# Kernel optimization log

Measured on AMD Instinct MI355X. Metric: run time of the kernel, lower is better.

## Reference

```python
import jax, jax.numpy as jnp
import numpy as np

ALPHA = 1.702
LIMIT = 7.0

# Tiling: A*B*M = BD*S (total dispatched tokens)
A, B, E, M, H, I = 2, 8, 16, 128, 2048, 2048
_BD, _S = 2, 1024


def setup_inputs() -> dict:
    key = jax.random.key(0)
    ks = jax.random.split(key, 6)
    inv_h = 1.0 / np.sqrt(H)
    inv_i = 1.0 / np.sqrt(I)
    return {
        "dispatched": jax.random.normal(ks[0], (A, B, E, M, H), dtype=jnp.float32),
        "gate_up_proj": jax.random.normal(ks[1], (E, H, 2 * I), dtype=jnp.float32) * inv_h,
        "gate_up_proj_bias": jax.random.normal(ks[2], (E, 2 * I), dtype=jnp.float32) * 0.02,
        "down_proj": jax.random.normal(ks[3], (E, I, H), dtype=jnp.float32) * inv_i,
        "down_proj_bias": jax.random.normal(ks[4], (E, H), dtype=jnp.float32) * 0.02,
        "sparsity_remap": jax.random.randint(ks[5], (E, E), 0, E, dtype=jnp.int32),
        "BD": _BD,
        "S": _S,
    }


def _moe_activation_gpt_oss(gate_up_out):
    # interleaved gate/up: [g0,u0,g1,u1,...]
    gate = gate_up_out[..., ::2]
    up = gate_up_out[..., 1::2]
    gate = jnp.minimum(gate, LIMIT)
    up = jnp.clip(up, -LIMIT, LIMIT)
    glu = gate * jax.nn.sigmoid(gate * ALPHA)
    return (up + 1.0) * glu


def reference(dispatched, gate_up_proj, gate_up_proj_bias, down_proj,
              down_proj_bias, sparsity_remap, BD, S):
    # sparsity_remap is an opaque tile remap for tt.sparse_matmul; the dense
    # grouped matmul computes the same math (zero tiles contribute zeros).
    a, b, e, m, h = dispatched.shape
    inter = gate_up_proj.shape[-1] // 2
    # grouped gate_up GEMM: [A,B,E,M,H] @ [E,H,2I] -> [A,B,E,M,2I]
    gate_up_out = jnp.einsum('abemh,ehn->abemn', dispatched, gate_up_proj)
    gate_up_out = gate_up_out + gate_up_proj_bias[None, None, :, None, :]
    activated = _moe_activation_gpt_oss(gate_up_out)  # [A,B,E,M,I]
    activated = activated.reshape(a * b, e, m, inter)
    # grouped down GEMM: [AB,E,M,I] @ [E,I,H] -> [AB,E,M,H]
    down_out = jnp.einsum('xemi,eih->xemh', activated, down_proj)
    down_out = down_out + down_proj_bias[None, :, None, :]
    # untile: [AB,E,M,H] -> [AB,M,E,H] -> [BD,S,E,H]
    down_out = jnp.transpose(down_out, (0, 2, 1, 3))
    return down_out.reshape(BD, S, e, h)
```

## Files before the change

### kernel.cpp

```cpp
#include <hip/hip_runtime.h>
#include <stdint.h>

#define DEV __device__ __forceinline__

constexpr int E_ = 16, M_ = 128, H_ = 2048, I_ = 2048;
constexpr int X_ = 16;
constexpr int N1 = 2 * I_;
constexpr int ROWS = X_ * M_;

typedef short bfrag __attribute__((ext_vector_type(8)));
typedef float ffrag __attribute__((ext_vector_type(4)));
typedef unsigned short us8 __attribute__((ext_vector_type(8)));

DEV unsigned short f2bf(float f) {
    union { float f; unsigned u; } v; v.f = f;
    unsigned u = v.u;
    u += 0x7fffu + ((u >> 16) & 1u);
    return (unsigned short)(u >> 16);
}

DEV void gload16(const void* g, void* lds_wave_base) {
    __builtin_amdgcn_global_load_lds(
        (const __attribute__((address_space(1))) unsigned int*)g,
        (__attribute__((address_space(3))) unsigned int*)lds_wave_base,
        16, 0, 0);
}

DEV void block_bar() {
    asm volatile("" ::: "memory");
    __builtin_amdgcn_s_barrier();
    asm volatile("" ::: "memory");
}


__global__ __launch_bounds__(256) void convert_a(const float* __restrict__ in,
                                                 unsigned short* __restrict__ outb) {
    const int n4 = X_ * E_ * M_ * H_ / 4;
    int idx = blockIdx.x * 256 + threadIdx.x;
    int stride = gridDim.x * 256;
    for (int f = idx; f < n4; f += stride) {
        float4 v = ((const float4*)in)[f];
        ushort4 o;
        o.x = f2bf(v.x); o.y = f2bf(v.y); o.z = f2bf(v.z); o.w = f2bf(v.w);
        const int c = f & 511;
        const int row = f >> 9;
        const int m = row & 127, e = (row >> 7) & 15, x = row >> 11;
        ((ushort4*)outb)[((size_t)(e * ROWS + x * M_ + m) << 9) + c] = o;
    }
}

__global__ __launch_bounds__(256) void convert_b1(const float* __restrict__ gup,
                                                  unsigned short* __restrict__ b1t) {
    const int e = blockIdx.x, h0 = blockIdx.y * 64, n0 = blockIdx.z * 128;
    __shared__ float tile[64][129];
    const float* src = gup + (size_t)e * H_ * N1;
    const int t = threadIdx.x;
#pragma unroll
    for (int i = 0; i < 8; ++i) {
        int idx = i * 1024 + t * 4;
        int r = idx >> 7, c = idx & 127;
        float4 v = *(const float4*)(src + (size_t)(h0 + r) * N1 + n0 + c);
        tile[r][c] = v.x; tile[r][c + 1] = v.y; tile[r][c + 2] = v.z; tile[r][c + 3] = v.w;
    }
    __syncthreads();
    const int p = t >> 2;
    const int hh = (t & 3) * 16;
    us8 g0, g1, u0, u1;
#pragma unroll
    for (int k = 0; k < 8; ++k) {
        g0[k] = f2bf(tile[hh + k][2 * p]);
        u0[k] = f2bf(tile[hh + k][2 * p + 1]);
        g1[k] = f2bf(tile[hh + 8 + k][2 * p]);
        u1[k] = f2bf(tile[hh + 8 + k][2 * p + 1]);
    }
    unsigned short* dg = b1t + ((size_t)e * N1 + (n0 >> 1) + p) * H_ + h0 + hh;
    unsigned short* du = b1t + ((size_t)e * N1 + I_ + (n0 >> 1) + p) * H_ + h0 + hh;
    *(us8*)dg = g0; *(us8*)(dg + 8) = g1;
    *(us8*)du = u0; *(us8*)(du + 8) = u1;
}

__global__ __launch_bounds__(256) void convert_b2(const float* __restrict__ dwn,
                                                  unsigned short* __restrict__ b2t) {
    const int e = blockIdx.x, i0 = blockIdx.y * 64, h0 = blockIdx.z * 64;
    __shared__ float tile[64][65];
    const float* src = dwn + (size_t)e * I_ * H_;
    const int t = threadIdx.x;
#pragma unroll
    for (int it = 0; it < 4; ++it) {
        int idx = it * 1024 + t * 4;
        int r = idx >> 6, c = idx & 63;
        float4 v = *(const float4*)(src + (size_t)(i0 + r) * H_ + h0 + c);
        tile[r][c] = v.x; tile[r][c + 1] = v.y; tile[r][c + 2] = v.z; tile[r][c + 3] = v.w;
    }
    __syncthreads();
    const int hl = t >> 2, ii = (t & 3) * 16;
    us8 o0, o1;
#pragma unroll
    for (int k = 0; k < 8; ++k) {
        o0[k] = f2bf(tile[ii + k][hl]);
        o1[k] = f2bf(tile[ii + 8 + k][hl]);
    }
    unsigned short* d = b2t + ((size_t)e * H_ + h0 + hl) * I_ + i0 + ii;
    *(us8*)d = o0; *(us8*)(d + 8) = o1;
}

template <int MODE>
__global__ __launch_bounds__(512, 2) void gemm8p(
    const unsigned short* __restrict__ A,
    const unsigned short* __restrict__ B,
    const float* __restrict__ bias,
    void* __restrict__ outv)
{
    constexpr int LD = 2048;
    constexpr int BK = 32;
    constexpr int NT = 2048 / BK;

    __shared__ unsigned short lds[4][2][256 * BK];

    const int t = threadIdx.x, wave = t >> 6, lane = t & 63;
    const int wr = wave >> 2, wc = wave & 3;

    int id = blockIdx.x;
    const int cpx = gridDim.x >> 3;
    id = (id & 7) * cpx + (id >> 3);
    int e, mt, bt;
    if (MODE == 0) { e = id >> 7; mt = (id >> 4) & 7; bt = id & 15; }
    else           { e = id >> 6; mt = (id >> 3) & 7; bt = id & 7; }

    const unsigned short* Aexp = A + ((size_t)e * ROWS + mt * 256) * LD;
    const unsigned short* Bexp = (MODE == 0)
        ? B + (size_t)e * N1 * LD
        : B + ((size_t)e * H_ + bt * 256) * LD;

    ffrag acc[8][4];
#pragma unroll
    for (int i = 0; i < 8; ++i)
#pragma unroll
        for (int j = 0; j < 4; ++j) acc[i][j] = ffrag{0.f, 0.f, 0.f, 0.f};

    const int rsub = lane >> 2;
    const int csw = ((lane & 3) ^ ((lane >> 3) & 3)) * 8;

    auto stage = [&](int kt, int b) {
        const int k0 = kt * BK;
#pragma unroll
        for (int i = 0; i < 2; ++i) {
            const int Rb = (wave * 2 + i) * 16;
            const int r = Rb + rsub;
            gload16(Aexp + (size_t)r * LD + k0 + csw, (void*)&lds[b][0][Rb * BK]);
        }
#pragma unroll
        for (int i = 0; i < 2; ++i) {
            const int Rb = (wave * 2 + i) * 16;
            const int r = Rb + rsub;
            int grow;
            if (MODE == 0)
                grow = ((r >> 5) & 1) * I_ + bt * 128 + (r >> 6) * 32 + (r & 31);
            else
                grow = r;
            gload16(Bexp + (size_t)grow * LD + k0 + csw, (void*)&lds[b][1][Rb * BK]);
        }
    };

    stage(0, 0);
    stage(1, 1);
    stage(2, 2);

    const int l15 = lane & 15, lr16 = lane >> 4;
    const int swl = (l15 >> 1) & 3;
    const int kch = (lr16 ^ swl) * 8;
    const int arow0 = wr * 128 + l15;
    const int brow0 = wc * 64 + l15;

#pragma unroll 4
    for (int kt = 0; kt < NT; ++kt) {
        const int cur = kt & 3;

        if (kt + 2 < NT)      { asm volatile("s_waitcnt vmcnt(8)" ::: "memory"); }
        else if (kt + 1 < NT) { asm volatile("s_waitcnt vmcnt(4)" ::: "memory"); }
        else                  { asm volatile("s_waitcnt vmcnt(0)" ::: "memory"); }
        __builtin_amdgcn_sched_barrier(0);
        block_bar();

        bfrag bB[4], af[8];

#pragma unroll
        for (int nf = 0; nf < 4; ++nf)
            bB[nf] = *(const bfrag*)&lds[cur][1][(brow0 + nf * 16) * BK + kch];
#pragma unroll
        for (int mf = 0; mf < 4; ++mf)
            af[mf] = *(const bfrag*)&lds[cur][0][(arow0 + mf * 16) * BK + kch];
        asm volatile("" ::: "memory");
#pragma unroll
        for (int mf = 4; mf < 8; ++mf)
            af[mf] = *(const bfrag*)&lds[cur][0][(arow0 + mf * 16) * BK + kch];

        if (kt + 3 < NT) stage(kt + 3, (kt + 3) & 3);

        asm volatile("s_waitcnt lgkmcnt(4)" ::: "memory");
        __builtin_amdgcn_sched_barrier(0);
        __builtin_amdgcn_s_setprio(1);
#pragma unroll
        for (int mf = 0; mf < 4; ++mf)
#pragma unroll
            for (int nf = 0; nf < 4; ++nf)
                acc[mf][nf] = __builtin_amdgcn_mfma_f32_16x16x32_bf16(
                    af[mf], bB[nf], acc[mf][nf], 0, 0, 0);
        __builtin_amdgcn_s_setprio(0);

        asm volatile("s_waitcnt lgkmcnt(0)" ::: "memory");
        __builtin_amdgcn_sched_barrier(0);
        __builtin_amdgcn_s_setprio(1);
#pragma unroll
        for (int mf = 4; mf < 8; ++mf)
#pragma unroll
            for (int nf = 0; nf < 4; ++nf)
                acc[mf][nf] = __builtin_amdgcn_mfma_f32_16x16x32_bf16(
                    af[mf], bB[nf], acc[mf][nf], 0, 0, 0);
        __builtin_amdgcn_s_setprio(0);
    }

    const int rb = mt * 256 + wr * 128 + lr16 * 4;
    if (MODE == 0) {
        unsigned short* act = (unsigned short*)outv + (size_t)e * ROWS * I_;
#pragma unroll
        for (int nf = 0; nf < 2; ++nf) {
            const int jj = bt * 128 + wc * 32 + nf * 16 + l15;
            const float gb = bias[(size_t)e * N1 + 2 * jj];
            const float ub = bias[(size_t)e * N1 + 2 * jj + 1];
#pragma unroll
            for (int mf = 0; mf < 8; ++mf)
#pragma unroll
                for (int r = 0; r < 4; ++r) {
                    float g = acc[mf][nf][r] + gb;
                    float u = acc[mf][2 + nf][r] + ub;
                    g = fminf(g, 7.0f);
                    u = fminf(fmaxf(u, -7.0f), 7.0f);
                    const float glu = g / (1.0f + __expf(-1.702f * g));
                    const float av = (u + 1.0f) * glu;
                    act[(size_t)(rb + mf * 16 + r) * I_ + jj] = f2bf(av);
                }
        }
    } else {
        float* out = (float*)outv;
#pragma unroll
        for (int nf = 0; nf < 4; ++nf) {
            const int h = bt * 256 + wc * 64 + nf * 16 + l15;
            const float bb = bias[(size_t)e * H_ + h];
#pragma unroll
            for (int mf = 0; mf < 8; ++mf)
#pragma unroll
                for (int r = 0; r < 4; ++r) {
                    const int row = rb + mf * 16 + r;
                    out[((size_t)row * E_ + e) * H_ + h] = acc[mf][nf][r] + bb;
                }
        }
    }
}


extern "C" void kernel_launch(void* const* d_in, const int* in_sizes, int n_in,
                              void* d_out, int out_size, void* d_ws, size_t ws_size,
                              hipStream_t stream) {
    const float* disp  = (const float*)d_in[0];
    const float* gup   = (const float*)d_in[1];
    const float* gub   = (const float*)d_in[2];
    const float* down  = (const float*)d_in[3];
    const float* dbias = (const float*)d_in[4];
    float* out = (float*)d_out;

    const size_t NEED = (size_t)512 << 20;
    if (ws_size < NEED) {
        hipMemsetAsync(d_out, 0, (size_t)out_size * sizeof(float), stream);
        return;
    }
    unsigned short* a_bf = (unsigned short*)d_ws;
    unsigned short* b1t  = (unsigned short*)((char*)d_ws + ((size_t)128 << 20));
    unsigned short* b2t  = b1t;
    unsigned short* actb = (unsigned short*)((char*)d_ws + ((size_t)384 << 20));

    convert_a<<<4096, 256, 0, stream>>>(disp, a_bf);
    convert_b1<<<dim3(E_, H_ / 64, N1 / 128), 256, 0, stream>>>(gup, b1t);
    gemm8p<0><<<2048, 512, 0, stream>>>(a_bf, b1t, gub, actb);
    convert_b2<<<dim3(E_, I_ / 64, H_ / 64), 256, 0, stream>>>(down, b2t);
    gemm8p<1><<<1024, 512, 0, stream>>>(actb, b2t, dbias, out);
}
```

Measured before the change: 1.185 ms.

## Software-pipeline LDS fragment loads across K tiles with ping-pong registers

Restructures the GEMM main loop so that the B fragments and the first half of the A fragments for the next K tile are read from LDS while the current tile's second MFMA half is running. Two register sets alternate between tiles, and the barrier and the next global stage move to the middle of each tile. The goal is to hide LDS read latency behind MFMA work. The cost is higher register pressure, and the loop is unrolled by two, which assumes NT is even.

```diff
diff --git a/kernel.cpp b/kernel.cpp
--- a/kernel.cpp
+++ b/kernel.cpp
@@ -162,63 +162,78 @@
         }
     };
 
-    stage(0, 0);
-    stage(1, 1);
-    stage(2, 2);
-
     const int l15 = lane & 15, lr16 = lane >> 4;
     const int swl = (l15 >> 1) & 3;
     const int kch = (lr16 ^ swl) * 8;
     const int arow0 = wr * 128 + l15;
     const int brow0 = wc * 64 + l15;
 
-#pragma unroll 4
-    for (int kt = 0; kt < NT; ++kt) {
-        const int cur = kt & 3;
-
-        if (kt + 2 < NT)      { asm volatile("s_waitcnt vmcnt(8)" ::: "memory"); }
-        else if (kt + 1 < NT) { asm volatile("s_waitcnt vmcnt(4)" ::: "memory"); }
-        else                  { asm volatile("s_waitcnt vmcnt(0)" ::: "memory"); }
-        __builtin_amdgcn_sched_barrier(0);
-        block_bar();
-
-        bfrag bB[4], af[8];
-
-#pragma unroll
-        for (int nf = 0; nf < 4; ++nf)
-            bB[nf] = *(const bfrag*)&lds[cur][1][(brow0 + nf * 16) * BK + kch];
-#pragma unroll
-        for (int mf = 0; mf < 4; ++mf)
-            af[mf] = *(const bfrag*)&lds[cur][0][(arow0 + mf * 16) * BK + kch];
-        asm volatile("" ::: "memory");
-#pragma unroll
-        for (int mf = 4; mf < 8; ++mf)
-            af[mf] = *(const bfrag*)&lds[cur][0][(arow0 + mf * 16) * BK + kch];
-
-        if (kt + 3 < NT) stage(kt + 3, (kt + 3) & 3);
-
-        asm volatile("s_waitcnt lgkmcnt(4)" ::: "memory");
-        __builtin_amdgcn_sched_barrier(0);
-        __builtin_amdgcn_s_setprio(1);
-#pragma unroll
-        for (int mf = 0; mf < 4; ++mf)
-#pragma unroll
-            for (int nf = 0; nf < 4; ++nf)
-                acc[mf][nf] = __builtin_amdgcn_mfma_f32_16x16x32_bf16(
-                    af[mf], bB[nf], acc[mf][nf], 0, 0, 0);
-        __builtin_amdgcn_s_setprio(0);
-
-        asm volatile("s_waitcnt lgkmcnt(0)" ::: "memory");
-        __builtin_amdgcn_sched_barrier(0);
-        __builtin_amdgcn_s_setprio(1);
-#pragma unroll
-        for (int mf = 4; mf < 8; ++mf)
-#pragma unroll
-            for (int nf = 0; nf < 4; ++nf)
-                acc[mf][nf] = __builtin_amdgcn_mfma_f32_16x16x32_bf16(
-                    af[mf], bB[nf], acc[mf][nf], 0, 0, 0);
-        __builtin_amdgcn_s_setprio(0);
-    }
+    bfrag bB_a[4], af_a[4], bB_b[4], af_b[4];
+
+    stage(0, 0);
+    stage(1, 1);
+    stage(2, 2);
+    asm volatile("s_waitcnt vmcnt(8)" ::: "memory");
+    __builtin_amdgcn_sched_barrier(0);
+    block_bar();
+#pragma unroll
+    for (int nf = 0; nf < 4; ++nf)
+        bB_a[nf] = *(const bfrag*)&lds[0][1][(brow0 + nf * 16) * BK + kch];
+#pragma unroll
+    for (int mf = 0; mf < 4; ++mf)
+        af_a[mf] = *(const bfrag*)&lds[0][0][(arow0 + mf * 16) * BK + kch];
+
+#define TILE_BODY(KT_, BBC, A03C, BBN, A03N)                                     \
+  {                                                                              \
+    const int kt_ = (KT_);                                                       \
+    const int cur_ = kt_ & 3;                                                    \
+    asm volatile("s_waitcnt lgkmcnt(0)" ::: "memory");      \
+    __builtin_amdgcn_sched_barrier(0);                                           \
+    bfrag af47[4];                                                               \
+    _Pragma("unroll")                                                            \
+    for (int mf = 0; mf < 4; ++mf)                                               \
+        af47[mf] = *(const bfrag*)&lds[cur_][0][(arow0 + (4 + mf) * 16) * BK + kch]; \
+    __builtin_amdgcn_sched_barrier(0);                                           \
+    __builtin_amdgcn_s_setprio(1);                                               \
+    _Pragma("unroll")                                                            \
+    for (int mf = 0; mf < 4; ++mf)                                               \
+        _Pragma("unroll")                                                        \
+        for (int nf = 0; nf < 4; ++nf)                                           \
+            acc[mf][nf] = __builtin_amdgcn_mfma_f32_16x16x32_bf16(               \
+                A03C[mf], BBC[nf], acc[mf][nf], 0, 0, 0);                        \
+    __builtin_amdgcn_s_setprio(0);                                               \
+    asm volatile("s_waitcnt lgkmcnt(0)" ::: "memory");          \
+    __builtin_amdgcn_sched_barrier(0);                                           \
+    if (kt_ + 1 < NT) {                                                          \
+        if (kt_ + 2 < NT) { asm volatile("s_waitcnt vmcnt(4)" ::: "memory"); }   \
+        else              { asm volatile("s_waitcnt vmcnt(0)" ::: "memory"); }   \
+        __builtin_amdgcn_sched_barrier(0);                                       \
+        block_bar();                             \
+        if (kt_ + 3 < NT) stage(kt_ + 3, (kt_ + 3) & 3);                         \
+        const int nxt_ = (kt_ + 1) & 3;                                          \
+        _Pragma("unroll")                                                        \
+        for (int nf = 0; nf < 4; ++nf)                                           \
+            BBN[nf] = *(const bfrag*)&lds[nxt_][1][(brow0 + nf * 16) * BK + kch]; \
+        _Pragma("unroll")                                                        \
+        for (int mf = 0; mf < 4; ++mf)                                           \
+            A03N[mf] = *(const bfrag*)&lds[nxt_][0][(arow0 + mf * 16) * BK + kch]; \
+        __builtin_amdgcn_sched_barrier(0);                                       \
+    }                                                                            \
+    __builtin_amdgcn_s_setprio(1);                                               \
+    _Pragma("unroll")                                                            \
+    for (int mf = 0; mf < 4; ++mf)                                               \
+        _Pragma("unroll")                                                        \
+        for (int nf = 0; nf < 4; ++nf)                                           \
+            acc[4 + mf][nf] = __builtin_amdgcn_mfma_f32_16x16x32_bf16(           \
+                af47[mf], BBC[nf], acc[4 + mf][nf], 0, 0, 0);                    \
+    __builtin_amdgcn_s_setprio(0);                                               \
+  }
+
+    for (int kt = 0; kt < NT; kt += 2) {
+        TILE_BODY(kt,     bB_a, af_a, bB_b, af_b);
+        TILE_BODY(kt + 1, bB_b, af_b, bB_a, af_a);
+    }
+#undef TILE_BODY
 
     const int rb = mt * 256 + wr * 128 + lr16 * 4;
     if (MODE == 0) {
```

After: 1.176 ms. About the same (-0.8%).

## Shrink GEMM tiles to 256x128 with 4 waves and double buffering

Applied to the files above, without the earlier changes.

Both grouped GEMMs move from 8-wave blocks with 256x256 tiles and a 4-stage LDS pipeline to 4-wave blocks with 256x128 tiles and a 2-stage double buffer. The grid doubles, and LDS per block shrinks, which may let more blocks share a CU. In exchange each block reuses loaded data less, the prefetch is only one stage deep, and a full vmcnt(0) wait runs every iteration, so memory latency is less hidden. convert_b1 also switches its LDS tile to float2 with vectorized float4 stores, which may cause bank conflicts where the padded layout avoided them.

```diff
diff --git a/kernel.cpp b/kernel.cpp
--- a/kernel.cpp
+++ b/kernel.cpp
@@ -52,7 +52,7 @@
 __global__ __launch_bounds__(256) void convert_b1(const float* __restrict__ gup,
                                                   unsigned short* __restrict__ b1t) {
     const int e = blockIdx.x, h0 = blockIdx.y * 64, n0 = blockIdx.z * 128;
-    __shared__ float tile[64][129];
+    __shared__ float2 tile2[64][64];
     const float* src = gup + (size_t)e * H_ * N1;
     const int t = threadIdx.x;
 #pragma unroll
@@ -60,7 +60,7 @@
         int idx = i * 1024 + t * 4;
         int r = idx >> 7, c = idx & 127;
         float4 v = *(const float4*)(src + (size_t)(h0 + r) * N1 + n0 + c);
-        tile[r][c] = v.x; tile[r][c + 1] = v.y; tile[r][c + 2] = v.z; tile[r][c + 3] = v.w;
+        *(float4*)&tile2[r][c >> 1] = v;
     }
     __syncthreads();
     const int p = t >> 2;
@@ -68,10 +68,10 @@
     us8 g0, g1, u0, u1;
 #pragma unroll
     for (int k = 0; k < 8; ++k) {
-        g0[k] = f2bf(tile[hh + k][2 * p]);
-        u0[k] = f2bf(tile[hh + k][2 * p + 1]);
-        g1[k] = f2bf(tile[hh + 8 + k][2 * p]);
-        u1[k] = f2bf(tile[hh + 8 + k][2 * p + 1]);
+        float2 a = tile2[hh + k][p];
+        float2 b = tile2[hh + 8 + k][p];
+        g0[k] = f2bf(a.x); u0[k] = f2bf(a.y);
+        g1[k] = f2bf(b.x); u1[k] = f2bf(b.y);
     }
     unsigned short* dg = b1t + ((size_t)e * N1 + (n0 >> 1) + p) * H_ + h0 + hh;
     unsigned short* du = b1t + ((size_t)e * N1 + I_ + (n0 >> 1) + p) * H_ + h0 + hh;
@@ -105,7 +105,7 @@
 }
 
 template <int MODE>
-__global__ __launch_bounds__(512, 2) void gemm8p(
+__global__ __launch_bounds__(256, 2) void gemm4w(
     const unsigned short* __restrict__ A,
     const unsigned short* __restrict__ B,
     const float* __restrict__ bias,
@@ -115,22 +115,23 @@
     constexpr int BK = 32;
     constexpr int NT = 2048 / BK;
 
-    __shared__ unsigned short lds[4][2][256 * BK];
+    __shared__ unsigned short ldsA[2][256 * BK];
+    __shared__ unsigned short ldsB[2][128 * BK];
 
     const int t = threadIdx.x, wave = t >> 6, lane = t & 63;
-    const int wr = wave >> 2, wc = wave & 3;
+    const int wr = wave >> 1, wc = wave & 1;
 
     int id = blockIdx.x;
     const int cpx = gridDim.x >> 3;
     id = (id & 7) * cpx + (id >> 3);
     int e, mt, bt;
-    if (MODE == 0) { e = id >> 7; mt = (id >> 4) & 7; bt = id & 15; }
-    else           { e = id >> 6; mt = (id >> 3) & 7; bt = id & 7; }
+    if (MODE == 0) { e = id >> 8; mt = (id >> 5) & 7; bt = id & 31; }
+    else           { e = id >> 7; mt = (id >> 4) & 7; bt = id & 15; }
 
     const unsigned short* Aexp = A + ((size_t)e * ROWS + mt * 256) * LD;
     const unsigned short* Bexp = (MODE == 0)
         ? B + (size_t)e * N1 * LD
-        : B + ((size_t)e * H_ + bt * 256) * LD;
+        : B + ((size_t)e * H_ + bt * 128) * LD;
 
     ffrag acc[8][4];
 #pragma unroll
@@ -144,10 +145,10 @@
     auto stage = [&](int kt, int b) {
         const int k0 = kt * BK;
 #pragma unroll
-        for (int i = 0; i < 2; ++i) {
-            const int Rb = (wave * 2 + i) * 16;
+        for (int i = 0; i < 4; ++i) {
+            const int Rb = (wave * 4 + i) * 16;
             const int r = Rb + rsub;
-            gload16(Aexp + (size_t)r * LD + k0 + csw, (void*)&lds[b][0][Rb * BK]);
+            gload16(Aexp + (size_t)r * LD + k0 + csw, (void*)&ldsA[b][Rb * BK]);
         }
 #pragma unroll
         for (int i = 0; i < 2; ++i) {
@@ -155,16 +156,14 @@
             const int r = Rb + rsub;
             int grow;
             if (MODE == 0)
-                grow = ((r >> 5) & 1) * I_ + bt * 128 + (r >> 6) * 32 + (r & 31);
+                grow = ((r >> 5) & 1) * I_ + bt * 64 + (r >> 6) * 32 + (r & 31);
             else
                 grow = r;
-            gload16(Bexp + (size_t)grow * LD + k0 + csw, (void*)&lds[b][1][Rb * BK]);
+            gload16(Bexp + (size_t)grow * LD + k0 + csw, (void*)&ldsB[b][Rb * BK]);
         }
     };
 
     stage(0, 0);
-    stage(1, 1);
-    stage(2, 2);
 
     const int l15 = lane & 15, lr16 = lane >> 4;
     const int swl = (l15 >> 1) & 3;
@@ -172,13 +171,11 @@
     const int arow0 = wr * 128 + l15;
     const int brow0 = wc * 64 + l15;
 
-#pragma unroll 4
+#pragma unroll 2
     for (int kt = 0; kt < NT; ++kt) {
-        const int cur = kt & 3;
-
-        if (kt + 2 < NT)      { asm volatile("s_waitcnt vmcnt(8)" ::: "memory"); }
-        else if (kt + 1 < NT) { asm volatile("s_waitcnt vmcnt(4)" ::: "memory"); }
-        else                  { asm volatile("s_waitcnt vmcnt(0)" ::: "memory"); }
+        const int cur = kt & 1;
+
+        asm volatile("s_waitcnt vmcnt(0)" ::: "memory");
         __builtin_amdgcn_sched_barrier(0);
         block_bar();
 
@@ -186,16 +183,16 @@
 
 #pragma unroll
         for (int nf = 0; nf < 4; ++nf)
-            bB[nf] = *(const bfrag*)&lds[cur][1][(brow0 + nf * 16) * BK + kch];
+            bB[nf] = *(const bfrag*)&ldsB[cur][(brow0 + nf * 16) * BK + kch];
 #pragma unroll
         for (int mf = 0; mf < 4; ++mf)
-            af[mf] = *(const bfrag*)&lds[cur][0][(arow0 + mf * 16) * BK + kch];
+            af[mf] = *(const bfrag*)&ldsA[cur][(arow0 + mf * 16) * BK + kch];
         asm volatile("" ::: "memory");
 #pragma unroll
         for (int mf = 4; mf < 8; ++mf)
-            af[mf] = *(const bfrag*)&lds[cur][0][(arow0 + mf * 16) * BK + kch];
-
-        if (kt + 3 < NT) stage(kt + 3, (kt + 3) & 3);
+            af[mf] = *(const bfrag*)&ldsA[cur][(arow0 + mf * 16) * BK + kch];
+
+        if (kt + 1 < NT) stage(kt + 1, cur ^ 1);
 
         asm volatile("s_waitcnt lgkmcnt(4)" ::: "memory");
         __builtin_amdgcn_sched_barrier(0);
@@ -225,7 +222,7 @@
         unsigned short* act = (unsigned short*)outv + (size_t)e * ROWS * I_;
 #pragma unroll
         for (int nf = 0; nf < 2; ++nf) {
-            const int jj = bt * 128 + wc * 32 + nf * 16 + l15;
+            const int jj = bt * 64 + wc * 32 + nf * 16 + l15;
             const float gb = bias[(size_t)e * N1 + 2 * jj];
             const float ub = bias[(size_t)e * N1 + 2 * jj + 1];
 #pragma unroll
@@ -245,7 +242,7 @@
         float* out = (float*)outv;
 #pragma unroll
         for (int nf = 0; nf < 4; ++nf) {
-            const int h = bt * 256 + wc * 64 + nf * 16 + l15;
+            const int h = bt * 128 + wc * 64 + nf * 16 + l15;
             const float bb = bias[(size_t)e * H_ + h];
 #pragma unroll
             for (int mf = 0; mf < 8; ++mf)
@@ -281,7 +278,7 @@
 
     convert_a<<<4096, 256, 0, stream>>>(disp, a_bf);
     convert_b1<<<dim3(E_, H_ / 64, N1 / 128), 256, 0, stream>>>(gup, b1t);
-    gemm8p<0><<<2048, 512, 0, stream>>>(a_bf, b1t, gub, actb);
+    gemm4w<0><<<4096, 256, 0, stream>>>(a_bf, b1t, gub, actb);
     convert_b2<<<dim3(E_, I_ / 64, H_ / 64), 256, 0, stream>>>(down, b2t);
-    gemm8p<1><<<1024, 512, 0, stream>>>(actb, b2t, dbias, out);
-}
+    gemm4w<1><<<2048, 256, 0, stream>>>(actb, b2t, dbias, out);
+}
```

New measurement: 1.261 ms, median of 2. 6.5% more time.
